# Kernel tuning notes

Hardware: AMD Instinct MI355X
Metric: run time of the kernel (lower is better)

## Reference

```python
import jax, jax.numpy as jnp
import numpy as np

B, S, E = 2, 1024, 1024
H, DH = 16, 64           # num_heads, key_dim = E // H
MAXLEN = 2048            # config.max_sequence_length -> table size 2*MAXLEN-1


def setup_inputs() -> dict:
    key = jax.random.key(0)
    ks = jax.random.split(key, 13)
    sc = 1.0 / np.sqrt(E)
    return {
        "query": jax.random.normal(ks[0], (B, S, E), jnp.float32),
        "key": jax.random.normal(ks[1], (B, S, E), jnp.float32),
        "value": jax.random.normal(ks[2], (B, S, E), jnp.float32),
        "Wq": jax.random.normal(ks[3], (E, E), jnp.float32) * sc,
        "bq": jnp.zeros((E,), jnp.float32),
        "Wk": jax.random.normal(ks[4], (E, E), jnp.float32) * sc,
        "bk": jnp.zeros((E,), jnp.float32),
        "Wv": jax.random.normal(ks[5], (E, E), jnp.float32) * sc,
        "bv": jnp.zeros((E,), jnp.float32),
        "Wo": jax.random.normal(ks[6], (E, E), jnp.float32) * sc,
        "bo": jnp.zeros((E,), jnp.float32),
        "rel_pos_emb": jax.random.normal(ks[7], (2 * MAXLEN - 1, DH), jnp.float32) * 0.02,
        "rel_pos_bias": jnp.zeros((2 * MAXLEN - 1,), jnp.float32),
    }


def _split_heads(x):
    # [B, S, E] -> [B, H, S, DH]
    return x.reshape(B, S, H, DH).transpose(0, 2, 1, 3)


def _relative_shift(x):
    # x: [B, H, S, S]; pad one zero column on the left of the last dim,
    # reshape to [B, H, S+1, S], drop the first row -> [B, H, S, S]
    x = jnp.pad(x, ((0, 0), (0, 0), (0, 0), (1, 0)))
    x = x.reshape(B, H, S + 1, S)
    return x[:, :, 1:, :]


def reference(query, key, value, Wq, bq, Wk, bk, Wv, bv, Wo, bo,
              rel_pos_emb, rel_pos_bias):
    q = _split_heads(query @ Wq + bq) / jnp.sqrt(jnp.float32(DH))  # [B,H,S,DH]
    k = _split_heads(key @ Wk + bk)                                 # [B,H,S,DH]
    v = _split_heads(value @ Wv + bv)                               # [B,H,S,DH]

    scores = jnp.einsum("bhid,bhjd->bhij", q, k)  # [B,H,S,S]

    # relative position term (gather + skew, as in the original call())
    pos_ids = jnp.arange(S)[:, None] - jnp.arange(S)[None, :] + (MAXLEN - 1)  # [S,S]
    rpe = rel_pos_emb[pos_ids]    # [S, S, DH]
    rpb = rel_pos_bias[pos_ids]   # [S, S]
    rel = jnp.einsum("bhid,ijd->bhij", q, rpe)  # [B,H,S,S]
    rel = _relative_shift(rel)
    scores = scores + rel + rpb   # rpb broadcasts over [B,H]

    weights = jax.nn.softmax(scores, axis=-1)
    out = jnp.einsum("bhij,bhjd->bhid", weights, v)  # [B,H,S,DH]
    out = out.transpose(0, 2, 1, 3).reshape(B, S, E)
    return out @ Wo + bo
```

## Files before the change

kernel.cpp:

```cpp
#include <hip/hip_runtime.h>

typedef unsigned short u16;
typedef __bf16 bf16_t;
typedef bf16_t bf16x8 __attribute__((ext_vector_type(8)));
typedef u16 u16x8 __attribute__((ext_vector_type(8)));
typedef float f32x4 __attribute__((ext_vector_type(4)));

#define DEVI __device__ __forceinline__


DEVI u16 f2bf(float f) {
    unsigned u = __builtin_bit_cast(unsigned, f);
    u = (u + 0x7FFFu + ((u >> 16) & 1u)) >> 16;
    return (u16)u;
}
DEVI float bf2f(u16 b) {
    unsigned u = ((unsigned)b) << 16;
    return __builtin_bit_cast(float, u);
}
DEVI f32x4 mfma16(u16x8 a, u16x8 b, f32x4 c) {
    return __builtin_amdgcn_mfma_f32_16x16x32_bf16(
        __builtin_bit_cast(bf16x8, a), __builtin_bit_cast(bf16x8, b), c, 0, 0, 0);
}
DEVI void gl2lds(const u16* g, u16* l) {
    __builtin_amdgcn_global_load_lds(
        (__attribute__((address_space(1))) void*)g,
        (__attribute__((address_space(3))) void*)l, 16, 0, 0);
}

__global__ __launch_bounds__(256) void cvt_kernel(
    const float* __restrict__ q, const float* __restrict__ k, const float* __restrict__ v,
    const float* __restrict__ emb,
    u16* __restrict__ xq, u16* __restrict__ xk, u16* __restrict__ xv, u16* __restrict__ embb)
{
    const long NQ = 2097152;
    const long NE = 262080;
    long i4 = ((long)blockIdx.x * 256 + threadIdx.x) * 4;
    if (i4 < 3 * NQ) {
        int which = (int)(i4 >> 21);
        long off = i4 & (NQ - 1);
        const float* src = which == 0 ? q : (which == 1 ? k : v);
        u16* dst = which == 0 ? xq : (which == 1 ? xk : xv);
        float4 f = *(const float4*)(src + off);
        ushort4 o; o.x = f2bf(f.x); o.y = f2bf(f.y); o.z = f2bf(f.z); o.w = f2bf(f.w);
        *(ushort4*)(dst + off) = o;
    } else {
        long off = i4 - 3 * NQ;
        if (off < NE) {
            float4 f = *(const float4*)(emb + off);
            ushort4 o; o.x = f2bf(f.x); o.y = f2bf(f.y); o.z = f2bf(f.z); o.w = f2bf(f.w);
            *(ushort4*)(embb + off) = o;
        }
    }
}

__global__ __launch_bounds__(256) void wt_kernel(
    const float* __restrict__ w0, const float* __restrict__ w1,
    const float* __restrict__ w2, const float* __restrict__ w3,
    u16* __restrict__ t0, u16* __restrict__ t1, u16* __restrict__ t2, u16* __restrict__ t3)
{
    int z = blockIdx.z;
    const float* W = z == 0 ? w0 : (z == 1 ? w1 : (z == 2 ? w2 : w3));
    u16* T = z == 0 ? t0 : (z == 1 ? t1 : (z == 2 ? t2 : t3));
    __shared__ float tile[64][65];
    int k0 = blockIdx.y * 64, n0 = blockIdx.x * 64;
    int tx = threadIdx.x, ty = threadIdx.y;
    for (int r = ty; r < 64; r += 4)
        tile[r][tx] = W[(long)(k0 + r) * 1024 + n0 + tx];
    __syncthreads();
    for (int r = ty; r < 64; r += 4)
        T[(long)(n0 + r) * 1024 + k0 + tx] = f2bf(tile[tx][r]);
}

template<int MT>
__global__ __launch_bounds__(256) void gemm_kernel(
    const u16* __restrict__ A0, const u16* __restrict__ A1, const u16* __restrict__ A2,
    const u16* __restrict__ W0, const u16* __restrict__ W1, const u16* __restrict__ W2,
    const float* __restrict__ bias0, const float* __restrict__ bias1, const float* __restrict__ bias2,
    u16* __restrict__ o0, u16* __restrict__ o1, u16* __restrict__ o2,
    float* __restrict__ ofp, int mode_base)
{
    int z = blockIdx.z;
    int mode = mode_base + z;
    const u16* A = z == 0 ? A0 : (z == 1 ? A1 : A2);
    const u16* W = z == 0 ? W0 : (z == 1 ? W1 : W2);
    const float* bias = z == 0 ? bias0 : (z == 1 ? bias1 : bias2);
    u16* ob = z == 0 ? o0 : (z == 1 ? o1 : o2);

    constexpr int MROWS = MT * 32;
    __shared__ u16 la[2 * MROWS * 32];
    __shared__ u16 lw[2 * 128 * 32];

    int lin = blockIdx.x + (blockIdx.y << 3);
    int xcd = lin & 7, idx = lin >> 3;
    int gy4 = gridDim.y >> 2;
    int xt = (xcd & 1) * 4 + (idx & 3);
    int yt = (xcd >> 1) * gy4 + (idx >> 2);
    int m0 = yt * MROWS, n0 = xt * 128;

    int t = threadIdx.x, lane = t & 63, wid = t >> 6;
    int l15 = lane & 15, quad = lane >> 4;
    int wm = (wid >> 1) * (MT * 16), wn = (wid & 1) * 64;
    int sr = lane >> 2, sp = lane & 3;

    f32x4 acc[MT][4] = {};

    auto stage = [&](int buf, int k0) {
        if constexpr (MT == 1) {
            if (wid < 2) {
                int r = wid * 16 + sr;
                int c = sp ^ ((r >> 1) & 3);
                gl2lds(A + (long)(m0 + r) * 1024 + k0 + c * 8,
                       la + buf * (MROWS * 32) + (wid * 16) * 32);
            }
        } else {
#pragma unroll
            for (int q = 0; q < MT / 2; q++) {
                int r = wid * (MT * 8) + q * 16 + sr;
                int c = sp ^ ((r >> 1) & 3);
                gl2lds(A + (long)(m0 + r) * 1024 + k0 + c * 8,
                       la + buf * (MROWS * 32) + (wid * (MT * 8) + q * 16) * 32);
            }
        }
#pragma unroll
        for (int q = 0; q < 2; q++) {
            int r = wid * 32 + q * 16 + sr;
            int c = sp ^ ((r >> 1) & 3);
            gl2lds(W + (long)(n0 + r) * 1024 + k0 + c * 8,
                   lw + buf * (128 * 32) + (wid * 32 + q * 16) * 32);
        }
    };

    stage(0, 0);
    __syncthreads();
    int cur = 0;
#pragma unroll 1
    for (int k0 = 0; k0 < 1024; k0 += 32) {
        if (k0 < 992) stage(cur ^ 1, k0 + 32);
        const u16* lab = la + cur * (MROWS * 32);
        const u16* lwb = lw + cur * (128 * 32);
        u16x8 af[MT], bfr[4];
#pragma unroll
        for (int mt = 0; mt < MT; mt++) {
            int r = wm + mt * 16 + l15;
            af[mt] = *(const u16x8*)&lab[r * 32 + ((quad ^ ((r >> 1) & 3)) * 8)];
        }
#pragma unroll
        for (int nt = 0; nt < 4; nt++) {
            int r = wn + nt * 16 + l15;
            bfr[nt] = *(const u16x8*)&lwb[r * 32 + ((quad ^ ((r >> 1) & 3)) * 8)];
        }
#pragma unroll
        for (int mt = 0; mt < MT; mt++)
#pragma unroll
            for (int nt = 0; nt < 4; nt++)
                acc[mt][nt] = mfma16(af[mt], bfr[nt], acc[mt][nt]);
        __syncthreads();
        cur ^= 1;
    }

#pragma unroll
    for (int mt = 0; mt < MT; mt++)
#pragma unroll
        for (int nt = 0; nt < 4; nt++)
#pragma unroll
            for (int reg = 0; reg < 4; reg++) {
                int gm = m0 + wm + mt * 16 + quad * 4 + reg;
                int gn = n0 + wn + nt * 16 + l15;
                float val = acc[mt][nt][reg] + bias[gn];
                if (mode == 0) {
                    val *= 0.125f;
                    long o = ((long)((gm >> 10) * 16 + (gn >> 6)) << 16) + ((gm & 1023) << 6) + (gn & 63);
                    ob[o] = f2bf(val);
                } else if (mode == 1) {
                    long o = ((long)((gm >> 10) * 16 + (gn >> 6)) << 16) + ((gm & 1023) << 6) + (gn & 63);
                    ob[o] = f2bf(val);
                } else if (mode == 2) {
                    long o = ((long)((gm >> 10) * 16 + (gn >> 6)) << 16) + ((long)(gn & 63) << 10) + (gm & 1023);
                    ob[o] = f2bf(val);
                } else {
                    ofp[(long)gm * 1024 + gn] = val;
                }
            }
}

__global__ __launch_bounds__(256) void gc_kernel(
    const u16* __restrict__ qb, const u16* __restrict__ embb,
    const float* __restrict__ rpb, u16* __restrict__ Bskew)
{
    int u0 = blockIdx.x * 32;
    int i0 = u0 & 1023;
    int t = threadIdx.x, lane = t & 63, wid = t >> 6;
    int l15 = lane & 15, quad = lane >> 4;

    __shared__ float lds_rpb[2048];
    for (int j = t; j < 1024; j += 256) {
        lds_rpb[j] = rpb[j + 2047];
        lds_rpb[1024 + j] = rpb[j + 1022];
    }
    __syncthreads();

    u16x8 aq[2][2];
#pragma unroll
    for (int rg = 0; rg < 2; rg++) {
        long qoff = (long)(u0 + rg * 16 + l15) * 64 + quad * 8;
        aq[rg][0] = *(const u16x8*)&qb[qoff];
        aq[rg][1] = *(const u16x8*)&qb[qoff + 32];
    }

    u16x8 nb0, nb1;
    {
        long ebase = (long)(1024 + i0 + wid * 16 + l15) * 64 + quad * 8;
        nb0 = *(const u16x8*)&embb[ebase];
        nb1 = *(const u16x8*)&embb[ebase + 32];
    }

    for (int tt = wid; tt < 66; tt += 4) {
        u16x8 b0 = nb0, b1 = nb1;
        if (tt + 4 < 66) {
            long ebase = (long)(1024 + i0 + (tt + 4) * 16 + l15) * 64 + quad * 8;
            nb0 = *(const u16x8*)&embb[ebase];
            nb1 = *(const u16x8*)&embb[ebase + 32];
        }
        int w0 = tt * 16;
#pragma unroll
        for (int rg = 0; rg < 2; rg++) {
            f32x4 c = {};
            c = mfma16(aq[rg][0], b0, c);
            c = mfma16(aq[rg][1], b1, c);
#pragma unroll
            for (int reg = 0; reg < 4; reg++) {
                int row = rg * 16 + quad * 4 + reg;
                int cc = w0 + l15 - row;
                if ((unsigned)cc <= 1023u) {
                    int i = i0 + row;
                    float rb = lds_rpb[cc + ((cc <= i) ? 0 : 1024)];
                    Bskew[((long)(u0 + row) << 10) + cc] = f2bf(c[reg] + rb);
                }
            }
        }
    }
}

__global__ __launch_bounds__(256, 4) void flash_kernel(
    const u16* __restrict__ qb, const u16* __restrict__ kb, const u16* __restrict__ vT,
    const u16* __restrict__ Bskew, const float* __restrict__ rpb,
    float* __restrict__ Po, float* __restrict__ Pm, float* __restrict__ Pl)
{
    int itile = blockIdx.x;
    int bh = blockIdx.y;
    int js = blockIdx.z;
    int t = threadIdx.x, lane = t & 63, wid = t >> 6;
    int l15 = lane & 15, quad = lane >> 4;
    int i0w = itile * 64 + wid * 16;

    __shared__ u16 lds_k[2][64 * 64];
    __shared__ u16 lds_v[2][64 * 64];
    __shared__ u16 lds_p[4][1024];

    int sr8 = lane >> 3, sp8 = lane & 7;

    float rpb2046 = rpb[2046];

    u16x8 aq[2];
    {
        long qoff = ((long)(bh * 1024) + i0w + l15) * 64 + quad * 8;
        aq[0] = *(const u16x8*)&qb[qoff];
        aq[1] = *(const u16x8*)&qb[qoff + 32];
    }
    float m_r[4], l_r[4];
    f32x4 o_acc[4] = {};
#pragma unroll
    for (int r = 0; r < 4; r++) { m_r[r] = -1e30f; l_r[r] = 0.f; }

    const u16* kbase = kb + (long)bh * 65536;
    const u16* vbase = vT + (long)bh * 65536;
    const u16* bbase = Bskew + ((long)bh << 20);

    auto stage = [&](int buf, int j0) {
#pragma unroll
        for (int q = 0; q < 2; q++) {
            int r = wid * 16 + q * 8 + sr8;
            int c = sp8 ^ (r & 7);
            gl2lds(kbase + (long)(j0 + r) * 64 + c * 8, &lds_k[buf][(wid * 16 + q * 8) * 64]);
            gl2lds(vbase + (long)r * 1024 + j0 + c * 8, &lds_v[buf][(wid * 16 + q * 8) * 64]);
        }
    };

    stage(0, js * 512);
    __syncthreads();
    int cur = 0;

#pragma unroll 1
    for (int jt = 0; jt < 8; jt++) {
        int j0 = js * 512 + jt * 64;
        if (jt < 7) stage(cur ^ 1, j0 + 64);

        f32x4 s_acc[4];
#pragma unroll
        for (int nt = 0; nt < 4; nt++) {
            int r = nt * 16 + l15;
            u16x8 b0 = *(const u16x8*)&lds_k[cur][r * 64 + ((quad ^ (r & 7)) * 8)];
            u16x8 b1 = *(const u16x8*)&lds_k[cur][r * 64 + (((quad + 4) ^ (r & 7)) * 8)];
            f32x4 c = {};
            c = mfma16(aq[0], b0, c);
            c = mfma16(aq[1], b1, c);
            s_acc[nt] = c;
        }

#pragma unroll
        for (int nt = 0; nt < 4; nt++) {
            int jn0 = j0 + nt * 16;
            int jj = jn0 + l15;
            if (jn0 + 15 <= i0w) {
#pragma unroll
                for (int reg = 0; reg < 4; reg++) {
                    int ii = i0w + quad * 4 + reg;
                    s_acc[nt][reg] += bf2f(bbase[((long)ii << 10) + (ii - jj)]);
                }
            } else if (jn0 >= i0w + 17) {
#pragma unroll
                for (int reg = 0; reg < 4; reg++) {
                    int ii = i0w + quad * 4 + reg;
                    s_acc[nt][reg] += bf2f(bbase[((long)(ii + 1) << 10) + (ii + 1025 - jj)]);
                }
            } else {
#pragma unroll
                for (int reg = 0; reg < 4; reg++) {
                    int ii = i0w + quad * 4 + reg;
                    float a;
                    if (jj <= ii)          a = bf2f(bbase[((long)ii << 10) + (ii - jj)]);
                    else if (jj == ii + 1) a = rpb2046;
                    else                   a = bf2f(bbase[((long)(ii + 1) << 10) + (ii + 1025 - jj)]);
                    s_acc[nt][reg] += a;
                }
            }
        }

#pragma unroll
        for (int reg = 0; reg < 4; reg++) {
            float mx = fmaxf(fmaxf(s_acc[0][reg], s_acc[1][reg]), fmaxf(s_acc[2][reg], s_acc[3][reg]));
            for (int off = 1; off < 16; off <<= 1) mx = fmaxf(mx, __shfl_xor(mx, off, 64));
            float mnew = fmaxf(m_r[reg], mx);
            float alpha = __expf(m_r[reg] - mnew);
            float rs = 0.f;
#pragma unroll
            for (int nt = 0; nt < 4; nt++) {
                float p = __expf(s_acc[nt][reg] - mnew);
                s_acc[nt][reg] = p;
                rs += p;
            }
            for (int off = 1; off < 16; off <<= 1) rs += __shfl_xor(rs, off, 64);
            l_r[reg] = l_r[reg] * alpha + rs;
            m_r[reg] = mnew;
#pragma unroll
            for (int dt = 0; dt < 4; dt++) o_acc[dt][reg] *= alpha;
        }

#pragma unroll
        for (int nt = 0; nt < 4; nt++)
#pragma unroll
            for (int reg = 0; reg < 4; reg++) {
                int row = quad * 4 + reg;
                int pos = ((nt * 2 + (l15 >> 3)) ^ (row & 7)) * 8 + (l15 & 7);
                lds_p[wid][row * 64 + pos] = f2bf(s_acc[nt][reg]);
            }

        u16x8 pf0 = *(const u16x8*)&lds_p[wid][l15 * 64 + ((quad ^ (l15 & 7)) * 8)];
        u16x8 pf1 = *(const u16x8*)&lds_p[wid][l15 * 64 + (((quad + 4) ^ (l15 & 7)) * 8)];
#pragma unroll
        for (int dt = 0; dt < 4; dt++) {
            int r = dt * 16 + l15;
            u16x8 v0 = *(const u16x8*)&lds_v[cur][r * 64 + ((quad ^ (r & 7)) * 8)];
            u16x8 v1 = *(const u16x8*)&lds_v[cur][r * 64 + (((quad + 4) ^ (r & 7)) * 8)];
            o_acc[dt] = mfma16(pf0, v0, o_acc[dt]);
            o_acc[dt] = mfma16(pf1, v1, o_acc[dt]);
        }

        __syncthreads();
        cur ^= 1;
    }

    int blk = (js * 32 + bh) * 16 + itile;
    float* PoB = Po + (long)blk * 4096;
#pragma unroll
    for (int dt = 0; dt < 4; dt++)
#pragma unroll
        for (int reg = 0; reg < 4; reg++) {
            int rr = wid * 16 + quad * 4 + reg;
            PoB[rr * 64 + dt * 16 + l15] = o_acc[dt][reg];
        }
    if (l15 == 0) {
#pragma unroll
        for (int reg = 0; reg < 4; reg++) {
            int rr = wid * 16 + quad * 4 + reg;
            Pm[blk * 64 + rr] = m_r[reg];
            Pl[blk * 64 + rr] = l_r[reg];
        }
    }
}

__global__ __launch_bounds__(256) void combine_kernel(
    const float* __restrict__ Po, const float* __restrict__ Pm, const float* __restrict__ Pl,
    u16* __restrict__ attn)
{
    int itile = blockIdx.x, bh = blockIdx.y;
    int t = threadIdx.x;
    int c = t & 63, rg = t >> 6;
    int blk0 = bh * 16 + itile;
    int blk1 = (32 + bh) * 16 + itile;
    int b = bh >> 4, h = bh & 15;
    for (int rr = rg; rr < 64; rr += 4) {
        float m0 = Pm[blk0 * 64 + rr], m1 = Pm[blk1 * 64 + rr];
        float ms = fmaxf(m0, m1);
        float e0 = __expf(m0 - ms), e1 = __expf(m1 - ms);
        float l = Pl[blk0 * 64 + rr] * e0 + Pl[blk1 * 64 + rr] * e1;
        float o = Po[(long)blk0 * 4096 + rr * 64 + c] * e0
                + Po[(long)blk1 * 4096 + rr * 64 + c] * e1;
        int ii = itile * 64 + rr;
        attn[((long)(b * 1024 + ii)) * 1024 + h * 64 + c] = f2bf(o / l);
    }
}

extern "C" void kernel_launch(void* const* d_in, const int* in_sizes, int n_in,
                              void* d_out, int out_size, void* d_ws, size_t ws_size,
                              hipStream_t stream)
{
    const float* query = (const float*)d_in[0];
    const float* key_  = (const float*)d_in[1];
    const float* value = (const float*)d_in[2];
    const float* Wq = (const float*)d_in[3];
    const float* bq = (const float*)d_in[4];
    const float* Wk = (const float*)d_in[5];
    const float* bk = (const float*)d_in[6];
    const float* Wv = (const float*)d_in[7];
    const float* bv = (const float*)d_in[8];
    const float* Wo = (const float*)d_in[9];
    const float* bo = (const float*)d_in[10];
    const float* emb = (const float*)d_in[11];
    const float* rpb = (const float*)d_in[12];

    char* ws = (char*)d_ws;
    u16* xq   = (u16*)(ws + 0);
    u16* xk   = (u16*)(ws + 4194304);
    u16* xv   = (u16*)(ws + 8388608);
    u16* WqT  = (u16*)(ws + 12582912);
    u16* WkT  = (u16*)(ws + 14680064);
    u16* WvT  = (u16*)(ws + 16777216);
    u16* embb = (u16*)(ws + 18874368);
    u16* WoT  = (u16*)(ws + 19922944);
    u16* qb   = (u16*)(ws + 22020096);
    u16* kb   = (u16*)(ws + 26214400);
    u16* vT   = (u16*)(ws + 30408704);
    u16* Bskew= (u16*)(ws + 34603008);
    float* Po = (float*)(ws + 0);
    float* Pm = (float*)(ws + 16777216);
    float* Pl = (float*)(ws + 17039360);
    u16* attn = (u16*)(ws + 22020096);

    cvt_kernel<<<6400, 256, 0, stream>>>(query, key_, value, emb, xq, xk, xv, embb);
    wt_kernel<<<dim3(16, 16, 4), dim3(64, 4), 0, stream>>>(Wq, Wk, Wv, Wo, WqT, WkT, WvT, WoT);
    gemm_kernel<2><<<dim3(8, 32, 3), 256, 0, stream>>>(xq, xk, xv, WqT, WkT, WvT,
                                                       bq, bk, bv, qb, kb, vT, nullptr, 0);
    gc_kernel<<<1024, 256, 0, stream>>>(qb, embb, rpb, Bskew);
    flash_kernel<<<dim3(16, 32, 2), 256, 0, stream>>>(qb, kb, vT, Bskew, rpb, Po, Pm, Pl);
    combine_kernel<<<dim3(16, 32), 256, 0, stream>>>(Po, Pm, Pl, attn);
    gemm_kernel<2><<<dim3(8, 32, 1), 256, 0, stream>>>(attn, nullptr, nullptr, WoT, nullptr, nullptr,
                                                       bo, nullptr, nullptr,
                                                       nullptr, nullptr, nullptr, (float*)d_out, 3);
}
```

Before: 245.0 us.

## Deepen GEMM K-step to 64, add lazy softmax rescale and MFMA priority hints

The projection GEMM now stages two 32-wide K slices per buffer and processes K=64 per loop iteration, halving the number of barriers. The attention kernel skips the running-max update and accumulator rescaling when no row's max grows by more than 8 (lazy rescale), which removes exp and multiply work. It also raises wave priority around the MFMA blocks. The MT==1 staging special case was removed, so an MT=1 instantiation would no longer stage A. Doubling LDS use may also reduce occupancy.

```diff
diff --git a/kernel.cpp b/kernel.cpp
--- a/kernel.cpp
+++ b/kernel.cpp
@@ -88,8 +88,8 @@
     u16* ob = z == 0 ? o0 : (z == 1 ? o1 : o2);
 
     constexpr int MROWS = MT * 32;
-    __shared__ u16 la[2 * MROWS * 32];
-    __shared__ u16 lw[2 * 128 * 32];
+    __shared__ u16 la[2 * 2 * MROWS * 32];
+    __shared__ u16 lw[2 * 2 * 128 * 32];
 
     int lin = blockIdx.x + (blockIdx.y << 3);
     int xcd = lin & 7, idx = lin >> 3;
@@ -105,56 +105,54 @@
 
     f32x4 acc[MT][4] = {};
 
-    auto stage = [&](int buf, int k0) {
-        if constexpr (MT == 1) {
-            if (wid < 2) {
-                int r = wid * 16 + sr;
-                int c = sp ^ ((r >> 1) & 3);
-                gl2lds(A + (long)(m0 + r) * 1024 + k0 + c * 8,
-                       la + buf * (MROWS * 32) + (wid * 16) * 32);
-            }
-        } else {
-#pragma unroll
-            for (int q = 0; q < MT / 2; q++) {
-                int r = wid * (MT * 8) + q * 16 + sr;
-                int c = sp ^ ((r >> 1) & 3);
-                gl2lds(A + (long)(m0 + r) * 1024 + k0 + c * 8,
-                       la + buf * (MROWS * 32) + (wid * (MT * 8) + q * 16) * 32);
-            }
+    auto stage_half = [&](int buf, int half, int k0) {
+#pragma unroll
+        for (int q = 0; q < MT / 2; q++) {
+            int r = wid * (MT * 8) + q * 16 + sr;
+            int c = sp ^ ((r >> 1) & 3);
+            gl2lds(A + (long)(m0 + r) * 1024 + k0 + c * 8,
+                   la + (buf * 2 + half) * (MROWS * 32) + (wid * (MT * 8) + q * 16) * 32);
         }
 #pragma unroll
         for (int q = 0; q < 2; q++) {
             int r = wid * 32 + q * 16 + sr;
             int c = sp ^ ((r >> 1) & 3);
             gl2lds(W + (long)(n0 + r) * 1024 + k0 + c * 8,
-                   lw + buf * (128 * 32) + (wid * 32 + q * 16) * 32);
-        }
+                   lw + (buf * 2 + half) * (128 * 32) + (wid * 32 + q * 16) * 32);
+        }
+    };
+    auto stage = [&](int buf, int k0) {
+        stage_half(buf, 0, k0);
+        stage_half(buf, 1, k0 + 32);
     };
 
     stage(0, 0);
     __syncthreads();
     int cur = 0;
 #pragma unroll 1
-    for (int k0 = 0; k0 < 1024; k0 += 32) {
-        if (k0 < 992) stage(cur ^ 1, k0 + 32);
-        const u16* lab = la + cur * (MROWS * 32);
-        const u16* lwb = lw + cur * (128 * 32);
-        u16x8 af[MT], bfr[4];
-#pragma unroll
-        for (int mt = 0; mt < MT; mt++) {
-            int r = wm + mt * 16 + l15;
-            af[mt] = *(const u16x8*)&lab[r * 32 + ((quad ^ ((r >> 1) & 3)) * 8)];
-        }
-#pragma unroll
-        for (int nt = 0; nt < 4; nt++) {
-            int r = wn + nt * 16 + l15;
-            bfr[nt] = *(const u16x8*)&lwb[r * 32 + ((quad ^ ((r >> 1) & 3)) * 8)];
-        }
-#pragma unroll
-        for (int mt = 0; mt < MT; mt++)
-#pragma unroll
-            for (int nt = 0; nt < 4; nt++)
-                acc[mt][nt] = mfma16(af[mt], bfr[nt], acc[mt][nt]);
+    for (int k0 = 0; k0 < 1024; k0 += 64) {
+        if (k0 < 960) stage(cur ^ 1, k0 + 64);
+#pragma unroll
+        for (int h = 0; h < 2; h++) {
+            const u16* lab = la + (cur * 2 + h) * (MROWS * 32);
+            const u16* lwb = lw + (cur * 2 + h) * (128 * 32);
+            u16x8 af[MT], bfr[4];
+#pragma unroll
+            for (int mt = 0; mt < MT; mt++) {
+                int r = wm + mt * 16 + l15;
+                af[mt] = *(const u16x8*)&lab[r * 32 + ((quad ^ ((r >> 1) & 3)) * 8)];
+            }
+#pragma unroll
+            for (int nt = 0; nt < 4; nt++) {
+                int r = wn + nt * 16 + l15;
+                bfr[nt] = *(const u16x8*)&lwb[r * 32 + ((quad ^ ((r >> 1) & 3)) * 8)];
+            }
+#pragma unroll
+            for (int mt = 0; mt < MT; mt++)
+#pragma unroll
+                for (int nt = 0; nt < 4; nt++)
+                    acc[mt][nt] = mfma16(af[mt], bfr[nt], acc[mt][nt]);
+        }
         __syncthreads();
         cur ^= 1;
     }
@@ -297,6 +295,7 @@
         if (jt < 7) stage(cur ^ 1, j0 + 64);
 
         f32x4 s_acc[4];
+        __builtin_amdgcn_s_setprio(1);
 #pragma unroll
         for (int nt = 0; nt < 4; nt++) {
             int r = nt * 16 + l15;
@@ -307,6 +306,7 @@
             c = mfma16(aq[1], b1, c);
             s_acc[nt] = c;
         }
+        __builtin_amdgcn_s_setprio(0);
 
 #pragma unroll
         for (int nt = 0; nt < 4; nt++) {
@@ -337,24 +337,46 @@
             }
         }
 
+        float mx[4];
 #pragma unroll
         for (int reg = 0; reg < 4; reg++) {
-            float mx = fmaxf(fmaxf(s_acc[0][reg], s_acc[1][reg]), fmaxf(s_acc[2][reg], s_acc[3][reg]));
-            for (int off = 1; off < 16; off <<= 1) mx = fmaxf(mx, __shfl_xor(mx, off, 64));
-            float mnew = fmaxf(m_r[reg], mx);
-            float alpha = __expf(m_r[reg] - mnew);
-            float rs = 0.f;
-#pragma unroll
-            for (int nt = 0; nt < 4; nt++) {
-                float p = __expf(s_acc[nt][reg] - mnew);
-                s_acc[nt][reg] = p;
-                rs += p;
-            }
-            for (int off = 1; off < 16; off <<= 1) rs += __shfl_xor(rs, off, 64);
-            l_r[reg] = l_r[reg] * alpha + rs;
-            m_r[reg] = mnew;
-#pragma unroll
-            for (int dt = 0; dt < 4; dt++) o_acc[dt][reg] *= alpha;
+            float m = fmaxf(fmaxf(s_acc[0][reg], s_acc[1][reg]), fmaxf(s_acc[2][reg], s_acc[3][reg]));
+            for (int off = 1; off < 16; off <<= 1) m = fmaxf(m, __shfl_xor(m, off, 64));
+            mx[reg] = m;
+        }
+        bool nogrow = (mx[0] <= m_r[0] + 8.f) && (mx[1] <= m_r[1] + 8.f) &&
+                      (mx[2] <= m_r[2] + 8.f) && (mx[3] <= m_r[3] + 8.f);
+        if (__all(nogrow)) {
+#pragma unroll
+            for (int reg = 0; reg < 4; reg++) {
+                float rs = 0.f;
+#pragma unroll
+                for (int nt = 0; nt < 4; nt++) {
+                    float p = __expf(s_acc[nt][reg] - m_r[reg]);
+                    s_acc[nt][reg] = p;
+                    rs += p;
+                }
+                for (int off = 1; off < 16; off <<= 1) rs += __shfl_xor(rs, off, 64);
+                l_r[reg] += rs;
+            }
+        } else {
+#pragma unroll
+            for (int reg = 0; reg < 4; reg++) {
+                float mnew = fmaxf(m_r[reg], mx[reg]);
+                float alpha = __expf(m_r[reg] - mnew);
+                float rs = 0.f;
+#pragma unroll
+                for (int nt = 0; nt < 4; nt++) {
+                    float p = __expf(s_acc[nt][reg] - mnew);
+                    s_acc[nt][reg] = p;
+                    rs += p;
+                }
+                for (int off = 1; off < 16; off <<= 1) rs += __shfl_xor(rs, off, 64);
+                l_r[reg] = l_r[reg] * alpha + rs;
+                m_r[reg] = mnew;
+#pragma unroll
+                for (int dt = 0; dt < 4; dt++) o_acc[dt][reg] *= alpha;
+            }
         }
 
 #pragma unroll
@@ -368,6 +390,7 @@
 
         u16x8 pf0 = *(const u16x8*)&lds_p[wid][l15 * 64 + ((quad ^ (l15 & 7)) * 8)];
         u16x8 pf1 = *(const u16x8*)&lds_p[wid][l15 * 64 + (((quad + 4) ^ (l15 & 7)) * 8)];
+        __builtin_amdgcn_s_setprio(1);
 #pragma unroll
         for (int dt = 0; dt < 4; dt++) {
             int r = dt * 16 + l15;
@@ -376,6 +399,7 @@
             o_acc[dt] = mfma16(pf0, v0, o_acc[dt]);
             o_acc[dt] = mfma16(pf1, v1, o_acc[dt]);
         }
+        __builtin_amdgcn_s_setprio(0);
 
         __syncthreads();
         cur ^= 1;
```

New measurement: 289.1 us. 1.18x slower.
